# Optimization experiments

Hardware: AMD Instinct MI355X
Metric: run time of the kernel (lower is better)

The kernel has to match this reference:

```python
import jax, jax.numpy as jnp
import numpy as np

DIM = 512
NUM_HEADS = 8
DIM_HEAD = 64
EPS = 1e-8
ROPE_THETA = 10000.0


def rms_norm(x, gamma):
    # F.normalize(x, dim=-1, p=2, eps) * sqrt(dim) * gamma
    norm = jnp.sqrt(jnp.sum(x * x, axis=-1, keepdims=True))
    x = x / jnp.maximum(norm, EPS)
    return x * (DIM ** 0.5) * gamma


def apply_rope(x):
    # x: [b, h, n, d], interleaved-pair RoPE (rotary-embedding-torch style)
    n, d = x.shape[-2], x.shape[-1]
    inv_freq = 1.0 / (ROPE_THETA ** (jnp.arange(0, d, 2, dtype=jnp.float32) / d))
    freqs = jnp.arange(n, dtype=jnp.float32)[:, None] * inv_freq[None, :]  # [n, d/2]
    freqs = jnp.repeat(freqs, 2, axis=-1)  # [n, d]
    cos, sin = jnp.cos(freqs), jnp.sin(freqs)
    x1 = x[..., ::2]
    x2 = x[..., 1::2]
    rot = jnp.stack((-x2, x1), axis=-1).reshape(x.shape)
    return x * cos + rot * sin


def setup_inputs() -> dict:
    key = jax.random.key(0)
    k1, k2, k3, k4 = jax.random.split(key, 4)
    b, n = 4, 2048
    dim_inner = NUM_HEADS * DIM_HEAD
    x = jax.random.normal(k1, (b, n, DIM), dtype=jnp.float32)
    gamma = jnp.ones((DIM,), dtype=jnp.float32)
    w_qkv = jax.random.normal(k2, (DIM, 3 * dim_inner), dtype=jnp.float32) * (DIM ** -0.5)
    w_out = jax.random.normal(k3, (dim_inner, DIM), dtype=jnp.float32) * (dim_inner ** -0.5)
    return {"x": x, "gamma": gamma, "w_qkv": w_qkv, "w_out": w_out}


def reference(x, gamma, w_qkv, w_out):
    b, n, _ = x.shape
    h, d = NUM_HEADS, DIM_HEAD
    xn = rms_norm(x, gamma)
    qkv = xn @ w_qkv  # [b, n, 3*h*d]
    qkv = qkv.reshape(b, n, 3, h, d)
    q = jnp.transpose(qkv[:, :, 0], (0, 2, 1, 3))  # [b, h, n, d]
    k = jnp.transpose(qkv[:, :, 1], (0, 2, 1, 3))
    v = jnp.transpose(qkv[:, :, 2], (0, 2, 1, 3))
    q = apply_rope(q)
    k = apply_rope(k)
    scale = d ** -0.5
    attn = jnp.einsum('bhnd,bhmd->bhnm', q, k) * scale
    attn = jax.nn.softmax(attn, axis=-1)
    out = jnp.einsum('bhnm,bhmd->bhnd', attn, v)
    out = jnp.transpose(out, (0, 2, 1, 3)).reshape(b, n, h * d)
    return out @ w_out
```

## Files before the change

kernel.cpp:

```cpp
#include <hip/hip_runtime.h>
#include <hip/hip_bf16.h>
#include <cmath>

#define B_SZ 4
#define N_SEQ 2048
#define DIM 512
#define NH 8
#define DH 64
#define QKV_N 1536
#define ROWS (B_SZ * N_SEQ)

typedef __bf16 bf16x8 __attribute__((ext_vector_type(8)));
typedef __bf16 bf16x4 __attribute__((ext_vector_type(4)));
typedef float  f32x4  __attribute__((ext_vector_type(4)));

#define GLOAD_LDS16(gp, lp)                                                     \
    __builtin_amdgcn_global_load_lds(                                           \
        (const __attribute__((address_space(1))) void*)(gp),                    \
        (__attribute__((address_space(3))) void*)(lp), 16, 0, 0)

#define MFMA_BF16 __builtin_amdgcn_mfma_f32_16x16x32_bf16

#define SBAR() asm volatile("s_barrier" ::: "memory")

__device__ __forceinline__ void tcast_tile(const float* __restrict__ W,
                                           __bf16* __restrict__ Wt,
                                           int K, int N, int n0, int k0, int t,
                                           float (*Ls)[68]) {
    const int tx = t & 15, ty = t >> 4;
    #pragma unroll
    for (int i = 0; i < 4; i++) {
        int k = ty + i * 16;
        float4 v = *(const float4*)&W[(size_t)(k0 + k) * N + n0 + tx * 4];
        *(float4*)&Ls[k][tx * 4] = v;
    }
    __syncthreads();
    const int nrow = t >> 2, seg = (t & 3) * 16;
    bf16x8 o0, o1;
    #pragma unroll
    for (int j = 0; j < 8; j++) o0[j] = (__bf16)Ls[seg + j][nrow];
    #pragma unroll
    for (int j = 0; j < 8; j++) o1[j] = (__bf16)Ls[seg + 8 + j][nrow];
    *(bf16x8*)&Wt[(size_t)(n0 + nrow) * K + k0 + seg]     = o0;
    *(bf16x8*)&Wt[(size_t)(n0 + nrow) * K + k0 + seg + 8] = o1;
}

__global__ __launch_bounds__(256) void prelude_kernel(const float* __restrict__ x,
                                                      const float* __restrict__ gamma,
                                                      const float* __restrict__ w_qkv,
                                                      const float* __restrict__ w_out,
                                                      __bf16* __restrict__ A,
                                                      __bf16* __restrict__ Wqkvt,
                                                      __bf16* __restrict__ Woutt) {
    __shared__ float Ls[64][68];
    const int bx = blockIdx.x, t = threadIdx.x;
    if (bx < 2048) {
        const int row  = bx * 4 + (t >> 6);
        const int lane = t & 63;
        const float4* xr = (const float4*)(x + (size_t)row * DIM);
        float4 a = xr[lane];
        float4 b = xr[lane + 64];
        float ss = a.x*a.x + a.y*a.y + a.z*a.z + a.w*a.w
                 + b.x*b.x + b.y*b.y + b.z*b.z + b.w*b.w;
        #pragma unroll
        for (int off = 32; off > 0; off >>= 1) ss += __shfl_xor(ss, off, 64);
        float s = 22.62741699796952f / fmaxf(sqrtf(ss), 1e-8f);
        const float4* gr = (const float4*)gamma;
        float4 g1 = gr[lane], g2 = gr[lane + 64];
        bf16x4 o1 = { (__bf16)(a.x*g1.x*s), (__bf16)(a.y*g1.y*s),
                      (__bf16)(a.z*g1.z*s), (__bf16)(a.w*g1.w*s) };
        bf16x4 o2 = { (__bf16)(b.x*g2.x*s), (__bf16)(b.y*g2.y*s),
                      (__bf16)(b.z*g2.z*s), (__bf16)(b.w*g2.w*s) };
        *(bf16x4*)(A + (size_t)row * DIM + lane * 4)       = o1;
        *(bf16x4*)(A + (size_t)row * DIM + 256 + lane * 4) = o2;
    } else {
        const int idx = bx - 2048;
        const int k0 = (idx >> 5) * 64, c = idx & 31;
        if (c < 24) tcast_tile(w_qkv, Wqkvt, DIM, QKV_N, c * 64, k0, t, Ls);
        else        tcast_tile(w_out, Woutt, DIM, DIM, (c - 24) * 64, k0, t, Ls);
    }
}

template <int N, typename OutT>
__global__ __launch_bounds__(256) void gemm_bf16_kernel(const __bf16* __restrict__ A,
                                                        const __bf16* __restrict__ Bt,
                                                        OutT* __restrict__ C) {
    __shared__ __bf16 As[128 * 32];
    __shared__ __bf16 Bs[128 * 32];
    const int t = threadIdx.x;
    const int lane = t & 63;
    const int w = t >> 6;
    const int l16 = lane & 15, quad = lane >> 4;
    const int wr = w >> 1, wc = w & 1;
    const int row0 = blockIdx.y * 128, col0 = blockIdx.x * 128;

    f32x4 acc[4][4] = {};

    const int r0a = t >> 2,         ks0 = (t & 3) * 8;
    const int r1a = (t + 256) >> 2, ks1 = (t & 3) * 8;

    for (int kt = 0; kt < DIM; kt += 32) {
        __syncthreads();
        GLOAD_LDS16(A  + (size_t)(row0 + r0a) * DIM + kt + ks0, As + t * 8);
        GLOAD_LDS16(A  + (size_t)(row0 + r1a) * DIM + kt + ks1, As + (t + 256) * 8);
        GLOAD_LDS16(Bt + (size_t)(col0 + r0a) * DIM + kt + ks0, Bs + t * 8);
        GLOAD_LDS16(Bt + (size_t)(col0 + r1a) * DIM + kt + ks1, Bs + (t + 256) * 8);
        __syncthreads();
        bf16x8 af[4], bfr[4];
        #pragma unroll
        for (int mi = 0; mi < 4; mi++)
            af[mi] = *(const bf16x8*)(As + (wr * 64 + mi * 16 + l16) * 32 + quad * 8);
        #pragma unroll
        for (int ni = 0; ni < 4; ni++)
            bfr[ni] = *(const bf16x8*)(Bs + (wc * 64 + ni * 16 + l16) * 32 + quad * 8);
        #pragma unroll
        for (int mi = 0; mi < 4; mi++)
            #pragma unroll
            for (int ni = 0; ni < 4; ni++)
                acc[mi][ni] = MFMA_BF16(af[mi], bfr[ni], acc[mi][ni], 0, 0, 0);
    }
    #pragma unroll
    for (int mi = 0; mi < 4; mi++) {
        #pragma unroll
        for (int ni = 0; ni < 4; ni++) {
            #pragma unroll
            for (int r = 0; r < 4; r++) {
                int m = row0 + wr * 64 + mi * 16 + quad * 4 + r;
                int n = col0 + wc * 64 + ni * 16 + l16;
                if constexpr (sizeof(OutT) == 4) {
                    C[(size_t)m * N + n] = acc[mi][ni][r];
                } else {
                    C[(size_t)m * N + n] = (__bf16)acc[mi][ni][r];
                }
            }
        }
    }
}

__global__ __launch_bounds__(256) void gemm_out_kernel(const __bf16* __restrict__ A,
                                                       const __bf16* __restrict__ Bt,
                                                       float* __restrict__ C) {
    __shared__ __bf16 As[64 * 32];
    __shared__ __bf16 Bs[128 * 32];
    const int t = threadIdx.x;
    const int lane = t & 63;
    const int w = t >> 6;
    const int l16 = lane & 15, quad = lane >> 4;
    const int wr = w >> 1, wc = w & 1;
    const int row0 = blockIdx.y * 64, col0 = blockIdx.x * 128;

    f32x4 acc[2][4] = {};

    const int r0a = t >> 2, ks0 = (t & 3) * 8;
    const int r1a = (t + 256) >> 2;

    for (int kt = 0; kt < DIM; kt += 32) {
        __syncthreads();
        GLOAD_LDS16(A  + (size_t)(row0 + r0a) * DIM + kt + ks0, As + t * 8);
        GLOAD_LDS16(Bt + (size_t)(col0 + r0a) * DIM + kt + ks0, Bs + t * 8);
        GLOAD_LDS16(Bt + (size_t)(col0 + r1a) * DIM + kt + ks0, Bs + (t + 256) * 8);
        __syncthreads();
        bf16x8 af[2], bfr[4];
        #pragma unroll
        for (int mi = 0; mi < 2; mi++)
            af[mi] = *(const bf16x8*)(As + (wr * 32 + mi * 16 + l16) * 32 + quad * 8);
        #pragma unroll
        for (int ni = 0; ni < 4; ni++)
            bfr[ni] = *(const bf16x8*)(Bs + (wc * 64 + ni * 16 + l16) * 32 + quad * 8);
        #pragma unroll
        for (int mi = 0; mi < 2; mi++)
            #pragma unroll
            for (int ni = 0; ni < 4; ni++)
                acc[mi][ni] = MFMA_BF16(af[mi], bfr[ni], acc[mi][ni], 0, 0, 0);
    }
    #pragma unroll
    for (int mi = 0; mi < 2; mi++)
        #pragma unroll
        for (int ni = 0; ni < 4; ni++)
            #pragma unroll
            for (int r = 0; r < 4; r++) {
                int m = row0 + wr * 32 + mi * 16 + quad * 4 + r;
                int n = col0 + wc * 64 + ni * 16 + l16;
                C[(size_t)m * 512 + n] = acc[mi][ni][r];
            }
}

__global__ __launch_bounds__(256) void prep_kernel(const __bf16* __restrict__ qkvb,
                                                   __bf16* __restrict__ Qb,
                                                   __bf16* __restrict__ Kf,
                                                   __bf16* __restrict__ Vf) {
    const int bx = blockIdx.x;
    const int nt = bx & 31;
    const int bh = bx >> 5;
    const int b  = bh >> 3;
    const int h  = bh & 7;
    const int t  = threadIdx.x;
    const float QSCALE = 0.18033688011112042f;

    {
        const int r  = t >> 2;
        const int d0 = (t & 3) << 4;
        const int pos = nt * 64 + r;
        const __bf16* qp = qkvb + (size_t)(b * N_SEQ + pos) * QKV_N + h * DH + d0;

        union Pack { __bf16 h[16]; uint4 u[2]; };
        Pack qi, ki, qo, ko;
        qi.u[0] = ((const uint4*)qp)[0];         qi.u[1] = ((const uint4*)qp)[1];
        ki.u[0] = ((const uint4*)(qp + 512))[0]; ki.u[1] = ((const uint4*)(qp + 512))[1];

        #pragma unroll
        for (int i = 0; i < 8; i++) {
            int p = (d0 >> 1) + i;
            float inv = exp2f(-0.41524101186092028f * (float)p);
            float ang = (float)pos * inv;
            float sn, cs;
            sincosf(ang, &sn, &cs);
            float qe = (float)qi.h[2*i], qd = (float)qi.h[2*i+1];
            float ke = (float)ki.h[2*i], kd = (float)ki.h[2*i+1];
            qo.h[2*i]   = (__bf16)(QSCALE * (qe * cs - qd * sn));
            qo.h[2*i+1] = (__bf16)(QSCALE * (qd * cs + qe * sn));
            ko.h[2*i]   = (__bf16)(ke * cs - kd * sn);
            ko.h[2*i+1] = (__bf16)(kd * cs + ke * sn);
        }
        uint4* qd_ = (uint4*)(Qb + ((size_t)bh * N_SEQ + pos) * DH + d0);
        qd_[0] = qo.u[0]; qd_[1] = qo.u[1];
        const int group = r >> 4, kl = r & 15;
        const int c = d0 >> 5, quad = (d0 & 31) >> 3;
        __bf16* kdst = Kf + ((size_t)bh * 32 + nt) * 4096
                          + (group * 2 + c) * 512 + (quad * 16 + kl) * 8;
        *(uint4*)kdst         = ko.u[0];
        *(uint4*)(kdst + 128) = ko.u[1];
    }

    {
        const int w = t >> 6, lane = t & 63;
        union PackV { __bf16 h[16]; unsigned long long q[4]; };
        PackV v;
        #pragma unroll
        for (int j = 0; j < 16; j++) {
            int row = nt * 64 + w * 16 + j;
            v.h[j] = qkvb[(size_t)(b * N_SEQ + row) * QKV_N + 1024 + h * DH + lane];
        }
        const int ng = lane >> 4, vl = lane & 15;
        __bf16* vdst = Vf + ((size_t)bh * 32 + nt) * 4096
                          + (ng * 2 + (w >> 1)) * 512 + vl * 8 + (w & 1) * 4;
        #pragma unroll
        for (int q = 0; q < 4; q++)
            *(unsigned long long*)(vdst + q * 128) = v.q[q];
    }
}

__global__ __launch_bounds__(256, 2) void attn_mfma_kernel(const __bf16* __restrict__ Qb,
                                                           const __bf16* __restrict__ Kf,
                                                           const __bf16* __restrict__ Vf,
                                                           __bf16* __restrict__ attn) {
    __shared__ __bf16 kv[2][2][8192];

    const int t    = threadIdx.x;
    const int w    = t >> 6;
    const int lane = t & 63;
    const int l16  = lane & 15;
    const int quad = lane >> 4;
    const int qh   = w >> 1;
    const int kp   = w & 1;

    const int bx = blockIdx.x;
    const int bh = bx & 31;
    const int qc = bx >> 5;
    const int b  = bh >> 3;
    const int h  = bh & 7;

    const int qrow0 = qc * 128 + qh * 64;
    const __bf16* Qh = Qb + ((size_t)bh * N_SEQ + qrow0) * DH;
    const __bf16* Kt = Kf + (size_t)bh * 32 * 4096;
    const __bf16* Vt = Vf + (size_t)bh * 32 * 4096;

    bf16x8 qa[4][2];
    #pragma unroll
    for (int f = 0; f < 4; f++) {
        qa[f][0] = *(const bf16x8*)(Qh + (size_t)(f * 16 + l16) * DH + quad * 8);
        qa[f][1] = *(const bf16x8*)(Qh + (size_t)(f * 16 + l16) * DH + 32 + quad * 8);
    }

    bf16x8 ones;
    #pragma unroll
    for (int i = 0; i < 8; i++) ones[i] = (__bf16)1.0f;

    f32x4 O[4][4] = {};
    f32x4 L[4] = {};

    auto dma_tile = [&](int tidx, int p, int pp) {
        const __bf16* kss = Kt + (size_t)tidx * 4096;
        const __bf16* vss = Vt + (size_t)tidx * 4096;
        __bf16* dst = &kv[p][pp][0];
        GLOAD_LDS16(kss + t * 8,        dst + t * 8);
        GLOAD_LDS16(kss + 2048 + t * 8, dst + 2048 + t * 8);
        GLOAD_LDS16(vss + t * 8,        dst + 4096 + t * 8);
        GLOAD_LDS16(vss + 2048 + t * 8, dst + 4096 + 2048 + t * 8);
    };

    dma_tile(0, 0, 0);
    dma_tile(1, 1, 0);
    for (int i = 0; i < 16; i++) {
        const int cur = i & 1;
        SBAR();
        if (i + 1 < 16) {
            dma_tile(2 * (i + 1),     0, cur ^ 1);
            dma_tile(2 * (i + 1) + 1, 1, cur ^ 1);
            asm volatile("s_waitcnt vmcnt(8)" ::: "memory");
        } else {
            asm volatile("s_waitcnt vmcnt(0)" ::: "memory");
        }
        SBAR();

        const __bf16* kb = &kv[kp][cur][0];
        const __bf16* vb = &kv[kp][cur][4096];

        bf16x8 kf[4][2];
        #pragma unroll
        for (int g = 0; g < 4; g++)
            #pragma unroll
            for (int c = 0; c < 2; c++)
                kf[g][c] = *(const bf16x8*)(kb + (g * 2 + c) * 512 + lane * 8);

        bf16x8 pa[4][2];
        #pragma unroll
        for (int f = 0; f < 4; f++) {
            f32x4 S[4];
            __builtin_amdgcn_s_setprio(1);
            #pragma unroll
            for (int g = 0; g < 4; g++) {
                f32x4 z = {0, 0, 0, 0};
                z = MFMA_BF16(kf[g][0], qa[f][0], z, 0, 0, 0);
                z = MFMA_BF16(kf[g][1], qa[f][1], z, 0, 0, 0);
                S[g] = z;
            }
            __builtin_amdgcn_s_setprio(0);
            #pragma unroll
            for (int j = 0; j < 8; j++) {
                pa[f][0][j] = (__bf16)__builtin_amdgcn_exp2f(S[(j >> 2)][j & 3]);
                pa[f][1][j] = (__bf16)__builtin_amdgcn_exp2f(S[2 + (j >> 2)][j & 3]);
            }
        }

        bf16x8 vf[4][2];
        #pragma unroll
        for (int n = 0; n < 4; n++)
            #pragma unroll
            for (int kc = 0; kc < 2; kc++)
                vf[n][kc] = *(const bf16x8*)(vb + (n * 2 + kc) * 512 + lane * 8);

        __builtin_amdgcn_s_setprio(1);
        #pragma unroll
        for (int f = 0; f < 4; f++) {
            #pragma unroll
            for (int n = 0; n < 4; n++) {
                O[f][n] = MFMA_BF16(pa[f][0], vf[n][0], O[f][n], 0, 0, 0);
                O[f][n] = MFMA_BF16(pa[f][1], vf[n][1], O[f][n], 0, 0, 0);
            }
            L[f] = MFMA_BF16(pa[f][0], ones, L[f], 0, 0, 0);
            L[f] = MFMA_BF16(pa[f][1], ones, L[f], 0, 0, 0);
        }
        __builtin_amdgcn_s_setprio(0);
    }

    __syncthreads();
    float* reds = (float*)&kv[0][0][0];
    float* myO = reds + (size_t)(qh * 64 + lane) * 68;
    float* myL = reds + 128 * 68 + (size_t)(qh * 64 + lane) * 20;
    if (kp == 1) {
        #pragma unroll
        for (int f = 0; f < 4; f++) {
            #pragma unroll
            for (int n = 0; n < 4; n++)
                *(f32x4*)(myO + (f * 4 + n) * 4) = O[f][n];
            *(f32x4*)(myL + f * 4) = L[f];
        }
    }
    __syncthreads();
    if (kp == 0) {
        #pragma unroll
        for (int f = 0; f < 4; f++) {
            #pragma unroll
            for (int n = 0; n < 4; n++)
                O[f][n] += *(const f32x4*)(myO + (f * 4 + n) * 4);
            L[f] += *(const f32x4*)(myL + f * 4);
        }
        #pragma unroll
        for (int f = 0; f < 4; f++) {
            float inv[4];
            #pragma unroll
            for (int r = 0; r < 4; r++) inv[r] = 1.0f / L[f][r];
            #pragma unroll
            for (int n = 0; n < 4; n++)
                #pragma unroll
                for (int r = 0; r < 4; r++) {
                    size_t row = (size_t)(b * N_SEQ + qrow0 + f * 16 + quad * 4 + r);
                    attn[row * 512 + h * DH + n * 16 + l16] =
                        (__bf16)(O[f][n][r] * inv[r]);
                }
        }
    }
}

extern "C" void kernel_launch(void* const* d_in, const int* in_sizes, int n_in,
                              void* d_out, int out_size, void* d_ws, size_t ws_size,
                              hipStream_t stream) {
    const float* x     = (const float*)d_in[0];
    const float* gamma = (const float*)d_in[1];
    const float* w_qkv = (const float*)d_in[2];
    const float* w_out = (const float*)d_in[3];
    float* out = (float*)d_out;

    __bf16* Abf   = (__bf16*)d_ws;
    __bf16* Wqkvt = Abf + (size_t)ROWS * DIM;
    __bf16* Woutt = Wqkvt + (size_t)QKV_N * DIM;
    __bf16* qkvb  = Woutt + (size_t)DIM * DIM;
    __bf16* attnb = qkvb;
    __bf16* Qb    = qkvb + (size_t)ROWS * QKV_N;
    __bf16* Kf    = Qb + (size_t)NH * B_SZ * N_SEQ * DH;
    __bf16* Vf    = Kf + (size_t)NH * B_SZ * N_SEQ * DH;

    prelude_kernel<<<2304, 256, 0, stream>>>(x, gamma, w_qkv, w_out,
                                             Abf, Wqkvt, Woutt);
    gemm_bf16_kernel<QKV_N, __bf16><<<dim3(QKV_N / 128, ROWS / 128), 256, 0, stream>>>(
        Abf, Wqkvt, qkvb);
    prep_kernel<<<1024, 256, 0, stream>>>(qkvb, Qb, Kf, Vf);
    attn_mfma_kernel<<<512, 256, 0, stream>>>(Qb, Kf, Vf, attnb);
    gemm_out_kernel<<<dim3(4, 128), 256, 0, stream>>>(attnb, Woutt, out);
}
```

Baseline: 151.6 us.

## Halve attention query tile, stream V from global, double occupancy

```diff
diff --git a/kernel.cpp b/kernel.cpp
--- a/kernel.cpp
+++ b/kernel.cpp
@@ -250,11 +250,11 @@
     }
 }
 
-__global__ __launch_bounds__(256, 2) void attn_mfma_kernel(const __bf16* __restrict__ Qb,
+__global__ __launch_bounds__(256, 4) void attn_mfma_kernel(const __bf16* __restrict__ Qb,
                                                            const __bf16* __restrict__ Kf,
                                                            const __bf16* __restrict__ Vf,
                                                            __bf16* __restrict__ attn) {
-    __shared__ __bf16 kv[2][2][8192];
+    __shared__ __bf16 kv[2][2][4096];
 
     const int t    = threadIdx.x;
     const int w    = t >> 6;
@@ -270,14 +270,14 @@
     const int b  = bh >> 3;
     const int h  = bh & 7;
 
-    const int qrow0 = qc * 128 + qh * 64;
+    const int qrow0 = qc * 64 + qh * 32;
     const __bf16* Qh = Qb + ((size_t)bh * N_SEQ + qrow0) * DH;
     const __bf16* Kt = Kf + (size_t)bh * 32 * 4096;
     const __bf16* Vt = Vf + (size_t)bh * 32 * 4096;
 
-    bf16x8 qa[4][2];
-    #pragma unroll
-    for (int f = 0; f < 4; f++) {
+    bf16x8 qa[2][2];
+    #pragma unroll
+    for (int f = 0; f < 2; f++) {
         qa[f][0] = *(const bf16x8*)(Qh + (size_t)(f * 16 + l16) * DH + quad * 8);
         qa[f][1] = *(const bf16x8*)(Qh + (size_t)(f * 16 + l16) * DH + 32 + quad * 8);
     }
@@ -286,36 +286,25 @@
     #pragma unroll
     for (int i = 0; i < 8; i++) ones[i] = (__bf16)1.0f;
 
-    f32x4 O[4][4] = {};
-    f32x4 L[4] = {};
-
-    auto dma_tile = [&](int tidx, int p, int pp) {
-        const __bf16* kss = Kt + (size_t)tidx * 4096;
-        const __bf16* vss = Vt + (size_t)tidx * 4096;
-        __bf16* dst = &kv[p][pp][0];
-        GLOAD_LDS16(kss + t * 8,        dst + t * 8);
-        GLOAD_LDS16(kss + 2048 + t * 8, dst + 2048 + t * 8);
-        GLOAD_LDS16(vss + t * 8,        dst + 4096 + t * 8);
-        GLOAD_LDS16(vss + 2048 + t * 8, dst + 4096 + 2048 + t * 8);
+    f32x4 O[2][4] = {};
+    f32x4 L[2] = {};
+
+    auto dma_pair = [&](int i, int pp) {
+        const __bf16* k0 = Kt + (size_t)(2 * i) * 4096;
+        const __bf16* k1 = Kt + (size_t)(2 * i + 1) * 4096;
+        GLOAD_LDS16(k0 + t * 8,        &kv[0][pp][t * 8]);
+        GLOAD_LDS16(k0 + 2048 + t * 8, &kv[0][pp][2048 + t * 8]);
+        GLOAD_LDS16(k1 + t * 8,        &kv[1][pp][t * 8]);
+        GLOAD_LDS16(k1 + 2048 + t * 8, &kv[1][pp][2048 + t * 8]);
     };
 
-    dma_tile(0, 0, 0);
-    dma_tile(1, 1, 0);
+    dma_pair(0, 0);
     for (int i = 0; i < 16; i++) {
         const int cur = i & 1;
+        asm volatile("s_waitcnt vmcnt(0)" ::: "memory");
         SBAR();
-        if (i + 1 < 16) {
-            dma_tile(2 * (i + 1),     0, cur ^ 1);
-            dma_tile(2 * (i + 1) + 1, 1, cur ^ 1);
-            asm volatile("s_waitcnt vmcnt(8)" ::: "memory");
-        } else {
-            asm volatile("s_waitcnt vmcnt(0)" ::: "memory");
-        }
-        SBAR();
 
         const __bf16* kb = &kv[kp][cur][0];
-        const __bf16* vb = &kv[kp][cur][4096];
-
         bf16x8 kf[4][2];
         #pragma unroll
         for (int g = 0; g < 4; g++)
@@ -323,36 +312,41 @@
             for (int c = 0; c < 2; c++)
                 kf[g][c] = *(const bf16x8*)(kb + (g * 2 + c) * 512 + lane * 8);
 
-        bf16x8 pa[4][2];
-        #pragma unroll
-        for (int f = 0; f < 4; f++) {
-            f32x4 S[4];
-            __builtin_amdgcn_s_setprio(1);
+        f32x4 S[2][4];
+        __builtin_amdgcn_s_setprio(1);
+        #pragma unroll
+        for (int f = 0; f < 2; f++)
             #pragma unroll
             for (int g = 0; g < 4; g++) {
                 f32x4 z = {0, 0, 0, 0};
                 z = MFMA_BF16(kf[g][0], qa[f][0], z, 0, 0, 0);
                 z = MFMA_BF16(kf[g][1], qa[f][1], z, 0, 0, 0);
-                S[g] = z;
+                S[f][g] = z;
             }
-            __builtin_amdgcn_s_setprio(0);
-            #pragma unroll
-            for (int j = 0; j < 8; j++) {
-                pa[f][0][j] = (__bf16)__builtin_amdgcn_exp2f(S[(j >> 2)][j & 3]);
-                pa[f][1][j] = (__bf16)__builtin_amdgcn_exp2f(S[2 + (j >> 2)][j & 3]);
-            }
-        }
-
+        __builtin_amdgcn_s_setprio(0);
+
+        const __bf16* vb = Vt + (size_t)(2 * i + kp) * 4096;
         bf16x8 vf[4][2];
         #pragma unroll
         for (int n = 0; n < 4; n++)
             #pragma unroll
             for (int kc = 0; kc < 2; kc++)
                 vf[n][kc] = *(const bf16x8*)(vb + (n * 2 + kc) * 512 + lane * 8);
+        asm volatile("" ::: "memory");
+        if (i + 1 < 16) dma_pair(i + 1, cur ^ 1);
+
+        bf16x8 pa[2][2];
+        #pragma unroll
+        for (int f = 0; f < 2; f++)
+            #pragma unroll
+            for (int j = 0; j < 8; j++) {
+                pa[f][0][j] = (__bf16)__builtin_amdgcn_exp2f(S[f][(j >> 2)][j & 3]);
+                pa[f][1][j] = (__bf16)__builtin_amdgcn_exp2f(S[f][2 + (j >> 2)][j & 3]);
+            }
 
         __builtin_amdgcn_s_setprio(1);
         #pragma unroll
-        for (int f = 0; f < 4; f++) {
+        for (int f = 0; f < 2; f++) {
             #pragma unroll
             for (int n = 0; n < 4; n++) {
                 O[f][n] = MFMA_BF16(pa[f][0], vf[n][0], O[f][n], 0, 0, 0);
@@ -366,11 +360,11 @@
 
     __syncthreads();
     float* reds = (float*)&kv[0][0][0];
-    float* myO = reds + (size_t)(qh * 64 + lane) * 68;
-    float* myL = reds + 128 * 68 + (size_t)(qh * 64 + lane) * 20;
+    float* myO = reds + (size_t)(qh * 64 + lane) * 36;
+    float* myL = reds + 4608 + (size_t)(qh * 64 + lane) * 12;
     if (kp == 1) {
         #pragma unroll
-        for (int f = 0; f < 4; f++) {
+        for (int f = 0; f < 2; f++) {
             #pragma unroll
             for (int n = 0; n < 4; n++)
                 *(f32x4*)(myO + (f * 4 + n) * 4) = O[f][n];
@@ -380,14 +374,14 @@
     __syncthreads();
     if (kp == 0) {
         #pragma unroll
-        for (int f = 0; f < 4; f++) {
+        for (int f = 0; f < 2; f++) {
             #pragma unroll
             for (int n = 0; n < 4; n++)
                 O[f][n] += *(const f32x4*)(myO + (f * 4 + n) * 4);
             L[f] += *(const f32x4*)(myL + f * 4);
         }
         #pragma unroll
-        for (int f = 0; f < 4; f++) {
+        for (int f = 0; f < 2; f++) {
             float inv[4];
             #pragma unroll
             for (int r = 0; r < 4; r++) inv[r] = 1.0f / L[f][r];
@@ -426,6 +420,6 @@
     gemm_bf16_kernel<QKV_N, __bf16><<<dim3(QKV_N / 128, ROWS / 128), 256, 0, stream>>>(
         Abf, Wqkvt, qkvb);
     prep_kernel<<<1024, 256, 0, stream>>>(qkvb, Qb, Kf, Vf);
-    attn_mfma_kernel<<<512, 256, 0, stream>>>(Qb, Kf, Vf, attnb);
+    attn_mfma_kernel<<<1024, 256, 0, stream>>>(Qb, Kf, Vf, attnb);
     gemm_out_kernel<<<dim3(4, 128), 256, 0, stream>>>(attnb, Woutt, out);
 }
```

Result: slower. 177.4 us (+17.0%).

## Fuse pipeline stages into two cooperative persistent kernels with grid syncs

Applied to the files above, without the earlier changes.

```diff
diff --git a/kernel.cpp b/kernel.cpp
--- a/kernel.cpp
+++ b/kernel.cpp
@@ -1,6 +1,9 @@
 #include <hip/hip_runtime.h>
 #include <hip/hip_bf16.h>
+#include <hip/hip_cooperative_groups.h>
 #include <cmath>
+
+namespace cg = cooperative_groups;
 
 #define B_SZ 4
 #define N_SEQ 2048
@@ -23,6 +26,29 @@
 
 #define SBAR() asm volatile("s_barrier" ::: "memory")
 
+__device__ __forceinline__ void rms_body(const float* __restrict__ x,
+                                         const float* __restrict__ gamma,
+                                         __bf16* __restrict__ A, int vb, int t) {
+    const int row  = vb * 4 + (t >> 6);
+    const int lane = t & 63;
+    const float4* xr = (const float4*)(x + (size_t)row * DIM);
+    float4 a = xr[lane];
+    float4 b = xr[lane + 64];
+    float ss = a.x*a.x + a.y*a.y + a.z*a.z + a.w*a.w
+             + b.x*b.x + b.y*b.y + b.z*b.z + b.w*b.w;
+    #pragma unroll
+    for (int off = 32; off > 0; off >>= 1) ss += __shfl_xor(ss, off, 64);
+    float s = 22.62741699796952f / fmaxf(sqrtf(ss), 1e-8f);
+    const float4* gr = (const float4*)gamma;
+    float4 g1 = gr[lane], g2 = gr[lane + 64];
+    bf16x4 o1 = { (__bf16)(a.x*g1.x*s), (__bf16)(a.y*g1.y*s),
+                  (__bf16)(a.z*g1.z*s), (__bf16)(a.w*g1.w*s) };
+    bf16x4 o2 = { (__bf16)(b.x*g2.x*s), (__bf16)(b.y*g2.y*s),
+                  (__bf16)(b.z*g2.z*s), (__bf16)(b.w*g2.w*s) };
+    *(bf16x4*)(A + (size_t)row * DIM + lane * 4)       = o1;
+    *(bf16x4*)(A + (size_t)row * DIM + 256 + lane * 4) = o2;
+}
+
 __device__ __forceinline__ void tcast_tile(const float* __restrict__ W,
                                            __bf16* __restrict__ Wt,
                                            int K, int N, int n0, int k0, int t,
@@ -45,57 +71,20 @@
     *(bf16x8*)&Wt[(size_t)(n0 + nrow) * K + k0 + seg + 8] = o1;
 }
 
-__global__ __launch_bounds__(256) void prelude_kernel(const float* __restrict__ x,
-                                                      const float* __restrict__ gamma,
-                                                      const float* __restrict__ w_qkv,
-                                                      const float* __restrict__ w_out,
-                                                      __bf16* __restrict__ A,
-                                                      __bf16* __restrict__ Wqkvt,
-                                                      __bf16* __restrict__ Woutt) {
-    __shared__ float Ls[64][68];
-    const int bx = blockIdx.x, t = threadIdx.x;
-    if (bx < 2048) {
-        const int row  = bx * 4 + (t >> 6);
-        const int lane = t & 63;
-        const float4* xr = (const float4*)(x + (size_t)row * DIM);
-        float4 a = xr[lane];
-        float4 b = xr[lane + 64];
-        float ss = a.x*a.x + a.y*a.y + a.z*a.z + a.w*a.w
-                 + b.x*b.x + b.y*b.y + b.z*b.z + b.w*b.w;
-        #pragma unroll
-        for (int off = 32; off > 0; off >>= 1) ss += __shfl_xor(ss, off, 64);
-        float s = 22.62741699796952f / fmaxf(sqrtf(ss), 1e-8f);
-        const float4* gr = (const float4*)gamma;
-        float4 g1 = gr[lane], g2 = gr[lane + 64];
-        bf16x4 o1 = { (__bf16)(a.x*g1.x*s), (__bf16)(a.y*g1.y*s),
-                      (__bf16)(a.z*g1.z*s), (__bf16)(a.w*g1.w*s) };
-        bf16x4 o2 = { (__bf16)(b.x*g2.x*s), (__bf16)(b.y*g2.y*s),
-                      (__bf16)(b.z*g2.z*s), (__bf16)(b.w*g2.w*s) };
-        *(bf16x4*)(A + (size_t)row * DIM + lane * 4)       = o1;
-        *(bf16x4*)(A + (size_t)row * DIM + 256 + lane * 4) = o2;
-    } else {
-        const int idx = bx - 2048;
-        const int k0 = (idx >> 5) * 64, c = idx & 31;
-        if (c < 24) tcast_tile(w_qkv, Wqkvt, DIM, QKV_N, c * 64, k0, t, Ls);
-        else        tcast_tile(w_out, Woutt, DIM, DIM, (c - 24) * 64, k0, t, Ls);
-    }
-}
-
 template <int N, typename OutT>
-__global__ __launch_bounds__(256) void gemm_bf16_kernel(const __bf16* __restrict__ A,
-                                                        const __bf16* __restrict__ Bt,
-                                                        OutT* __restrict__ C) {
-    __shared__ __bf16 As[128 * 32];
-    __shared__ __bf16 Bs[128 * 32];
+__device__ __forceinline__ void gemm128x128(const __bf16* __restrict__ A,
+                                            const __bf16* __restrict__ Bt,
+                                            OutT* __restrict__ C,
+                                            int row0, int col0, char* smraw) {
+    __bf16* As = (__bf16*)smraw;
+    __bf16* Bs = (__bf16*)(smraw + 8192);
     const int t = threadIdx.x;
     const int lane = t & 63;
     const int w = t >> 6;
     const int l16 = lane & 15, quad = lane >> 4;
     const int wr = w >> 1, wc = w & 1;
-    const int row0 = blockIdx.y * 128, col0 = blockIdx.x * 128;
 
     f32x4 acc[4][4] = {};
-
     const int r0a = t >> 2,         ks0 = (t & 3) * 8;
     const int r1a = (t + 256) >> 2, ks1 = (t & 3) * 8;
 
@@ -120,37 +109,32 @@
                 acc[mi][ni] = MFMA_BF16(af[mi], bfr[ni], acc[mi][ni], 0, 0, 0);
     }
     #pragma unroll
-    for (int mi = 0; mi < 4; mi++) {
-        #pragma unroll
-        for (int ni = 0; ni < 4; ni++) {
+    for (int mi = 0; mi < 4; mi++)
+        #pragma unroll
+        for (int ni = 0; ni < 4; ni++)
             #pragma unroll
             for (int r = 0; r < 4; r++) {
                 int m = row0 + wr * 64 + mi * 16 + quad * 4 + r;
                 int n = col0 + wc * 64 + ni * 16 + l16;
-                if constexpr (sizeof(OutT) == 4) {
-                    C[(size_t)m * N + n] = acc[mi][ni][r];
-                } else {
-                    C[(size_t)m * N + n] = (__bf16)acc[mi][ni][r];
-                }
+                if constexpr (sizeof(OutT) == 4) C[(size_t)m * N + n] = acc[mi][ni][r];
+                else                             C[(size_t)m * N + n] = (__bf16)acc[mi][ni][r];
             }
-        }
-    }
-}
-
-__global__ __launch_bounds__(256) void gemm_out_kernel(const __bf16* __restrict__ A,
-                                                       const __bf16* __restrict__ Bt,
-                                                       float* __restrict__ C) {
-    __shared__ __bf16 As[64 * 32];
-    __shared__ __bf16 Bs[128 * 32];
+}
+
+template <int N, typename OutT>
+__device__ __forceinline__ void gemm64x128(const __bf16* __restrict__ A,
+                                           const __bf16* __restrict__ Bt,
+                                           OutT* __restrict__ C,
+                                           int row0, int col0, char* smraw) {
+    __bf16* As = (__bf16*)smraw;
+    __bf16* Bs = (__bf16*)(smraw + 4096);
     const int t = threadIdx.x;
     const int lane = t & 63;
     const int w = t >> 6;
     const int l16 = lane & 15, quad = lane >> 4;
     const int wr = w >> 1, wc = w & 1;
-    const int row0 = blockIdx.y * 64, col0 = blockIdx.x * 128;
 
     f32x4 acc[2][4] = {};
-
     const int r0a = t >> 2, ks0 = (t & 3) * 8;
     const int r1a = (t + 256) >> 2;
 
@@ -181,20 +165,20 @@
             for (int r = 0; r < 4; r++) {
                 int m = row0 + wr * 32 + mi * 16 + quad * 4 + r;
                 int n = col0 + wc * 64 + ni * 16 + l16;
-                C[(size_t)m * 512 + n] = acc[mi][ni][r];
+                if constexpr (sizeof(OutT) == 4) C[(size_t)m * N + n] = acc[mi][ni][r];
+                else                             C[(size_t)m * N + n] = (__bf16)acc[mi][ni][r];
             }
 }
 
-__global__ __launch_bounds__(256) void prep_kernel(const __bf16* __restrict__ qkvb,
-                                                   __bf16* __restrict__ Qb,
-                                                   __bf16* __restrict__ Kf,
-                                                   __bf16* __restrict__ Vf) {
-    const int bx = blockIdx.x;
+__device__ __forceinline__ void prep_body(const __bf16* __restrict__ qkvb,
+                                          __bf16* __restrict__ Qb,
+                                          __bf16* __restrict__ Kf,
+                                          __bf16* __restrict__ Vf,
+                                          int bx, int t) {
     const int nt = bx & 31;
     const int bh = bx >> 5;
     const int b  = bh >> 3;
     const int h  = bh & 7;
-    const int t  = threadIdx.x;
     const float QSCALE = 0.18033688011112042f;
 
     {
@@ -250,13 +234,13 @@
     }
 }
 
-__global__ __launch_bounds__(256, 2) void attn_mfma_kernel(const __bf16* __restrict__ Qb,
-                                                           const __bf16* __restrict__ Kf,
-                                                           const __bf16* __restrict__ Vf,
-                                                           __bf16* __restrict__ attn) {
-    __shared__ __bf16 kv[2][2][8192];
-
-    const int t    = threadIdx.x;
+__device__ __forceinline__ void attn_body(const __bf16* __restrict__ Qb,
+                                          const __bf16* __restrict__ Kf,
+                                          const __bf16* __restrict__ Vf,
+                                          __bf16* __restrict__ attn,
+                                          int bx, int t, char* smraw) {
+    __bf16 (*kv)[2][8192] = reinterpret_cast<__bf16 (*)[2][8192]>(smraw);
+
     const int w    = t >> 6;
     const int lane = t & 63;
     const int l16  = lane & 15;
@@ -264,7 +248,6 @@
     const int qh   = w >> 1;
     const int kp   = w & 1;
 
-    const int bx = blockIdx.x;
     const int bh = bx & 31;
     const int qc = bx >> 5;
     const int b  = bh >> 3;
@@ -365,7 +348,7 @@
     }
 
     __syncthreads();
-    float* reds = (float*)&kv[0][0][0];
+    float* reds = (float*)smraw;
     float* myO = reds + (size_t)(qh * 64 + lane) * 68;
     float* myL = reds + 128 * 68 + (size_t)(qh * 64 + lane) * 20;
     if (kp == 1) {
@@ -401,6 +384,104 @@
                 }
         }
     }
+}
+
+__global__ __launch_bounds__(256) void prelude_kernel(const float* __restrict__ x,
+                                                      const float* __restrict__ gamma,
+                                                      const float* __restrict__ w_qkv,
+                                                      const float* __restrict__ w_out,
+                                                      __bf16* __restrict__ A,
+                                                      __bf16* __restrict__ Wqkvt,
+                                                      __bf16* __restrict__ Woutt) {
+    __shared__ float Ls[64][68];
+    const int bx = blockIdx.x, t = threadIdx.x;
+    if (bx < 2048) {
+        rms_body(x, gamma, A, bx, t);
+    } else {
+        const int idx = bx - 2048;
+        const int k0 = (idx >> 5) * 64, c = idx & 31;
+        if (c < 24) tcast_tile(w_qkv, Wqkvt, DIM, QKV_N, c * 64, k0, t, Ls);
+        else        tcast_tile(w_out, Woutt, DIM, DIM, (c - 24) * 64, k0, t, Ls);
+    }
+}
+
+__global__ __launch_bounds__(256) void gemm_qkv_kernel(const __bf16* __restrict__ A,
+                                                       const __bf16* __restrict__ Bt,
+                                                       __bf16* __restrict__ C) {
+    __shared__ __align__(16) char sm[16384];
+    gemm128x128<QKV_N, __bf16>(A, Bt, C, blockIdx.y * 128, blockIdx.x * 128, sm);
+}
+
+__global__ __launch_bounds__(256) void prep_kernel(const __bf16* __restrict__ qkvb,
+                                                   __bf16* __restrict__ Qb,
+                                                   __bf16* __restrict__ Kf,
+                                                   __bf16* __restrict__ Vf) {
+    prep_body(qkvb, Qb, Kf, Vf, blockIdx.x, threadIdx.x);
+}
+
+__global__ __launch_bounds__(256, 2) void attn_mfma_kernel(const __bf16* __restrict__ Qb,
+                                                           const __bf16* __restrict__ Kf,
+                                                           const __bf16* __restrict__ Vf,
+                                                           __bf16* __restrict__ attn) {
+    __shared__ __align__(16) char sm[65536];
+    attn_body(Qb, Kf, Vf, attn, blockIdx.x, threadIdx.x, sm);
+}
+
+__global__ __launch_bounds__(256) void gemm_out_kernel(const __bf16* __restrict__ A,
+                                                       const __bf16* __restrict__ Bt,
+                                                       float* __restrict__ C) {
+    __shared__ __align__(16) char sm[12288];
+    gemm64x128<DIM, float>(A, Bt, C, blockIdx.y * 64, blockIdx.x * 128, sm);
+}
+
+__global__ __launch_bounds__(256, 2) void mega1(const float* __restrict__ x,
+                                                const float* __restrict__ gamma,
+                                                const float* __restrict__ w_qkv,
+                                                const float* __restrict__ w_out,
+                                                __bf16* __restrict__ Abf,
+                                                __bf16* __restrict__ Wqkvt,
+                                                __bf16* __restrict__ Woutt,
+                                                __bf16* __restrict__ qkvb,
+                                                __bf16* __restrict__ Qb,
+                                                __bf16* __restrict__ Kf,
+                                                __bf16* __restrict__ Vf) {
+    __shared__ __align__(16) char sm[17408];
+    cg::grid_group grid = cg::this_grid();
+    const int bid = blockIdx.x, t = threadIdx.x;
+
+    for (int vb = bid; vb < 2304; vb += 512) {
+        if (vb < 2048) {
+            rms_body(x, gamma, Abf, vb, t);
+        } else {
+            const int idx = vb - 2048;
+            float (*Ls)[68] = reinterpret_cast<float (*)[68]>(sm);
+            const int k0 = (idx >> 5) * 64, c = idx & 31;
+            if (c < 24) tcast_tile(w_qkv, Wqkvt, DIM, QKV_N, c * 64, k0, t, Ls);
+            else        tcast_tile(w_out, Woutt, DIM, DIM, (c - 24) * 64, k0, t, Ls);
+        }
+    }
+    grid.sync();
+
+    for (int vb = bid; vb < 768; vb += 512)
+        gemm128x128<QKV_N, __bf16>(Abf, Wqkvt, qkvb, (vb / 12) * 128, (vb % 12) * 128, sm);
+    grid.sync();
+
+    for (int vb = bid; vb < 1024; vb += 512)
+        prep_body(qkvb, Qb, Kf, Vf, vb, t);
+}
+
+__global__ __launch_bounds__(256, 2) void mega2(const __bf16* __restrict__ Qb,
+                                                const __bf16* __restrict__ Kf,
+                                                const __bf16* __restrict__ Vf,
+                                                __bf16* __restrict__ attnb,
+                                                const __bf16* __restrict__ Woutt,
+                                                float* __restrict__ out) {
+    __shared__ __align__(16) char sm[65536];
+    cg::grid_group grid = cg::this_grid();
+    attn_body(Qb, Kf, Vf, attnb, blockIdx.x, threadIdx.x, sm);
+    grid.sync();
+    const int vb = blockIdx.x;
+    gemm64x128<DIM, float>(attnb, Woutt, out, (vb >> 2) * 64, (vb & 3) * 128, sm);
 }
 
 extern "C" void kernel_launch(void* const* d_in, const int* in_sizes, int n_in,
@@ -421,11 +502,28 @@
     __bf16* Kf    = Qb + (size_t)NH * B_SZ * N_SEQ * DH;
     __bf16* Vf    = Kf + (size_t)NH * B_SZ * N_SEQ * DH;
 
-    prelude_kernel<<<2304, 256, 0, stream>>>(x, gamma, w_qkv, w_out,
-                                             Abf, Wqkvt, Woutt);
-    gemm_bf16_kernel<QKV_N, __bf16><<<dim3(QKV_N / 128, ROWS / 128), 256, 0, stream>>>(
-        Abf, Wqkvt, qkvb);
-    prep_kernel<<<1024, 256, 0, stream>>>(qkvb, Qb, Kf, Vf);
-    attn_mfma_kernel<<<512, 256, 0, stream>>>(Qb, Kf, Vf, attnb);
-    gemm_out_kernel<<<dim3(4, 128), 256, 0, stream>>>(attnb, Woutt, out);
-}
+    void* a1[] = { (void*)&x, (void*)&gamma, (void*)&w_qkv, (void*)&w_out,
+                   (void*)&Abf, (void*)&Wqkvt, (void*)&Woutt, (void*)&qkvb,
+                   (void*)&Qb, (void*)&Kf, (void*)&Vf };
+    void* a2[] = { (void*)&Qb, (void*)&Kf, (void*)&Vf, (void*)&attnb,
+                   (void*)&Woutt, (void*)&out };
+
+    bool m1 = hipLaunchCooperativeKernel(reinterpret_cast<void*>(mega1),
+                                         dim3(512), dim3(256), a1, 0, stream)
+              == hipSuccess;
+    if (!m1) {
+        prelude_kernel<<<2304, 256, 0, stream>>>(x, gamma, w_qkv, w_out,
+                                                 Abf, Wqkvt, Woutt);
+        gemm_qkv_kernel<<<dim3(QKV_N / 128, ROWS / 128), 256, 0, stream>>>(
+            Abf, Wqkvt, qkvb);
+        prep_kernel<<<1024, 256, 0, stream>>>(qkvb, Qb, Kf, Vf);
+    }
+
+    bool m2 = m1 && hipLaunchCooperativeKernel(reinterpret_cast<void*>(mega2),
+                                               dim3(512), dim3(256), a2, 0, stream)
+                    == hipSuccess;
+    if (!m2) {
+        attn_mfma_kernel<<<512, 256, 0, stream>>>(Qb, Kf, Vf, attnb);
+        gemm_out_kernel<<<dim3(4, 128), 256, 0, stream>>>(attnb, Woutt, out);
+    }
+}
```

New measurement: 379.2 us. 2.5x slower.

## Double-buffer LDS tiles in QKV and output GEMMs to overlap loads with MFMA

Applied to the files above, without the earlier changes.

```diff
diff --git a/kernel.cpp b/kernel.cpp
--- a/kernel.cpp
+++ b/kernel.cpp
@@ -85,8 +85,8 @@
 __global__ __launch_bounds__(256) void gemm_bf16_kernel(const __bf16* __restrict__ A,
                                                         const __bf16* __restrict__ Bt,
                                                         OutT* __restrict__ C) {
-    __shared__ __bf16 As[128 * 32];
-    __shared__ __bf16 Bs[128 * 32];
+    __shared__ __bf16 As[2][128 * 32];
+    __shared__ __bf16 Bs[2][128 * 32];
     const int t = threadIdx.x;
     const int lane = t & 63;
     const int w = t >> 6;
@@ -97,27 +97,42 @@
     f32x4 acc[4][4] = {};
 
     const int r0a = t >> 2,         ks0 = (t & 3) * 8;
-    const int r1a = (t + 256) >> 2, ks1 = (t & 3) * 8;
-
-    for (int kt = 0; kt < DIM; kt += 32) {
-        __syncthreads();
-        GLOAD_LDS16(A  + (size_t)(row0 + r0a) * DIM + kt + ks0, As + t * 8);
-        GLOAD_LDS16(A  + (size_t)(row0 + r1a) * DIM + kt + ks1, As + (t + 256) * 8);
-        GLOAD_LDS16(Bt + (size_t)(col0 + r0a) * DIM + kt + ks0, Bs + t * 8);
-        GLOAD_LDS16(Bt + (size_t)(col0 + r1a) * DIM + kt + ks1, Bs + (t + 256) * 8);
-        __syncthreads();
+    const int r1a = (t + 256) >> 2;
+
+    auto dma = [&](int kidx, int bb) {
+        const int kt = kidx * 32;
+        GLOAD_LDS16(A  + (size_t)(row0 + r0a) * DIM + kt + ks0, As[bb] + t * 8);
+        GLOAD_LDS16(A  + (size_t)(row0 + r1a) * DIM + kt + ks0, As[bb] + (t + 256) * 8);
+        GLOAD_LDS16(Bt + (size_t)(col0 + r0a) * DIM + kt + ks0, Bs[bb] + t * 8);
+        GLOAD_LDS16(Bt + (size_t)(col0 + r1a) * DIM + kt + ks0, Bs[bb] + (t + 256) * 8);
+    };
+
+    dma(0, 0);
+    for (int i = 0; i < 16; i++) {
+        const int cur = i & 1;
+        SBAR();
+        if (i + 1 < 16) {
+            dma(i + 1, cur ^ 1);
+            asm volatile("s_waitcnt vmcnt(4)" ::: "memory");
+        } else {
+            asm volatile("s_waitcnt vmcnt(0)" ::: "memory");
+        }
+        SBAR();
+
         bf16x8 af[4], bfr[4];
         #pragma unroll
         for (int mi = 0; mi < 4; mi++)
-            af[mi] = *(const bf16x8*)(As + (wr * 64 + mi * 16 + l16) * 32 + quad * 8);
+            af[mi] = *(const bf16x8*)(As[cur] + (wr * 64 + mi * 16 + l16) * 32 + quad * 8);
         #pragma unroll
         for (int ni = 0; ni < 4; ni++)
-            bfr[ni] = *(const bf16x8*)(Bs + (wc * 64 + ni * 16 + l16) * 32 + quad * 8);
+            bfr[ni] = *(const bf16x8*)(Bs[cur] + (wc * 64 + ni * 16 + l16) * 32 + quad * 8);
+        __builtin_amdgcn_s_setprio(1);
         #pragma unroll
         for (int mi = 0; mi < 4; mi++)
             #pragma unroll
             for (int ni = 0; ni < 4; ni++)
                 acc[mi][ni] = MFMA_BF16(af[mi], bfr[ni], acc[mi][ni], 0, 0, 0);
+        __builtin_amdgcn_s_setprio(0);
     }
     #pragma unroll
     for (int mi = 0; mi < 4; mi++) {
@@ -140,8 +155,8 @@
 __global__ __launch_bounds__(256) void gemm_out_kernel(const __bf16* __restrict__ A,
                                                        const __bf16* __restrict__ Bt,
                                                        float* __restrict__ C) {
-    __shared__ __bf16 As[64 * 32];
-    __shared__ __bf16 Bs[128 * 32];
+    __shared__ __bf16 As[2][64 * 32];
+    __shared__ __bf16 Bs[2][128 * 32];
     const int t = threadIdx.x;
     const int lane = t & 63;
     const int w = t >> 6;
@@ -154,24 +169,39 @@
     const int r0a = t >> 2, ks0 = (t & 3) * 8;
     const int r1a = (t + 256) >> 2;
 
-    for (int kt = 0; kt < DIM; kt += 32) {
-        __syncthreads();
-        GLOAD_LDS16(A  + (size_t)(row0 + r0a) * DIM + kt + ks0, As + t * 8);
-        GLOAD_LDS16(Bt + (size_t)(col0 + r0a) * DIM + kt + ks0, Bs + t * 8);
-        GLOAD_LDS16(Bt + (size_t)(col0 + r1a) * DIM + kt + ks0, Bs + (t + 256) * 8);
-        __syncthreads();
+    auto dma = [&](int kidx, int bb) {
+        const int kt = kidx * 32;
+        GLOAD_LDS16(A  + (size_t)(row0 + r0a) * DIM + kt + ks0, As[bb] + t * 8);
+        GLOAD_LDS16(Bt + (size_t)(col0 + r0a) * DIM + kt + ks0, Bs[bb] + t * 8);
+        GLOAD_LDS16(Bt + (size_t)(col0 + r1a) * DIM + kt + ks0, Bs[bb] + (t + 256) * 8);
+    };
+
+    dma(0, 0);
+    for (int i = 0; i < 16; i++) {
+        const int cur = i & 1;
+        SBAR();
+        if (i + 1 < 16) {
+            dma(i + 1, cur ^ 1);
+            asm volatile("s_waitcnt vmcnt(3)" ::: "memory");
+        } else {
+            asm volatile("s_waitcnt vmcnt(0)" ::: "memory");
+        }
+        SBAR();
+
         bf16x8 af[2], bfr[4];
         #pragma unroll
         for (int mi = 0; mi < 2; mi++)
-            af[mi] = *(const bf16x8*)(As + (wr * 32 + mi * 16 + l16) * 32 + quad * 8);
+            af[mi] = *(const bf16x8*)(As[cur] + (wr * 32 + mi * 16 + l16) * 32 + quad * 8);
         #pragma unroll
         for (int ni = 0; ni < 4; ni++)
-            bfr[ni] = *(const bf16x8*)(Bs + (wc * 64 + ni * 16 + l16) * 32 + quad * 8);
+            bfr[ni] = *(const bf16x8*)(Bs[cur] + (wc * 64 + ni * 16 + l16) * 32 + quad * 8);
+        __builtin_amdgcn_s_setprio(1);
         #pragma unroll
         for (int mi = 0; mi < 2; mi++)
             #pragma unroll
             for (int ni = 0; ni < 4; ni++)
                 acc[mi][ni] = MFMA_BF16(af[mi], bfr[ni], acc[mi][ni], 0, 0, 0);
+        __builtin_amdgcn_s_setprio(0);
     }
     #pragma unroll
     for (int mi = 0; mi < 2; mi++)
```

Result: no change. 153.1 us (+1.0%).
